# Kernel tuning notes

Hardware: AMD Instinct MI355X
Metric: run time of the kernel (lower is better)

Reference implementation:

```python
import jax, jax.numpy as jnp
import numpy as np

NUM_HEAD = 8
MSA_DIM = 256
PAIR_DIM = 128
KEY_DIM = MSA_DIM // NUM_HEAD  # 32 per-head dim
LN_EPS = 1e-5


def _layernorm(x, scale, offset):
    mu = jnp.mean(x, axis=-1, keepdims=True)
    var = jnp.var(x, axis=-1, keepdims=True)
    return (x - mu) * jax.lax.rsqrt(var + LN_EPS) * scale + offset


def setup_inputs() -> dict:
    key = jax.random.key(0)
    ks = jax.random.split(key, 16)
    S, R = 256, 256  # num sequences, num residues
    inp = {
        "msa_act": jax.random.normal(ks[0], (S, R, MSA_DIM), dtype=jnp.float32),
        "msa_mask": jnp.ones((S, R), dtype=jnp.int32),
        "pair_act": jax.random.normal(ks[1], (R, R, PAIR_DIM), dtype=jnp.float32),
        # LayerNorm params
        "qn_scale": jax.random.normal(ks[2], (MSA_DIM,), dtype=jnp.float32) * 0.02 + 1.0,
        "qn_offset": jax.random.normal(ks[3], (MSA_DIM,), dtype=jnp.float32) * 0.02,
        "pn_scale": jax.random.normal(ks[4], (PAIR_DIM,), dtype=jnp.float32) * 0.02 + 1.0,
        "pn_offset": jax.random.normal(ks[5], (PAIR_DIM,), dtype=jnp.float32) * 0.02,
        # pair-bias projection
        "feat_2d_weights": jax.random.normal(ks[6], (PAIR_DIM, NUM_HEAD), dtype=jnp.float32) * 0.1,
        # attention params
        "q_weights": jax.random.normal(ks[7], (MSA_DIM, NUM_HEAD, KEY_DIM), dtype=jnp.float32) * 0.05,
        "k_weights": jax.random.normal(ks[8], (MSA_DIM, NUM_HEAD, KEY_DIM), dtype=jnp.float32) * 0.05,
        "v_weights": jax.random.normal(ks[9], (MSA_DIM, NUM_HEAD, KEY_DIM), dtype=jnp.float32) * 0.05,
        "o_weights": jax.random.normal(ks[10], (NUM_HEAD, KEY_DIM, MSA_DIM), dtype=jnp.float32) * 0.05,
        "o_bias": jnp.zeros((MSA_DIM,), dtype=jnp.float32),
        "gating_w": jax.random.normal(ks[11], (MSA_DIM, NUM_HEAD, KEY_DIM), dtype=jnp.float32) * 0.05,
        "gating_b": jnp.ones((NUM_HEAD, KEY_DIM), dtype=jnp.float32),
    }
    return inp


def reference(msa_act, msa_mask, pair_act, qn_scale, qn_offset, pn_scale, pn_offset,
              feat_2d_weights, q_weights, k_weights, v_weights, o_weights, o_bias,
              gating_w, gating_b):
    # mask bias: [S, 1, 1, R]
    bias = (1e9 * (msa_mask.astype(jnp.float32) - 1.0))[:, None, None, :]
    m = _layernorm(msa_act, qn_scale, qn_offset)            # [S, R, C]
    p = _layernorm(pair_act, pn_scale, pn_offset)           # [R, R, Cz]
    nonbatched_bias = jnp.einsum('qkc,ch->hqk', p, feat_2d_weights)  # [H, R, R]

    q = jnp.einsum('bqa,ahc->bqhc', m, q_weights) * (KEY_DIM ** -0.5)
    k = jnp.einsum('bka,ahc->bkhc', m, k_weights)
    v = jnp.einsum('bka,ahc->bkhc', m, v_weights)
    logits = jnp.einsum('bqhc,bkhc->bhqk', q, k) + bias + nonbatched_bias[None]
    weights = jax.nn.softmax(logits, axis=-1)
    weighted_avg = jnp.einsum('bhqk,bkhc->bqhc', weights, v)

    gate = jax.nn.sigmoid(jnp.einsum('bqc,chv->bqhv', m, gating_w) + gating_b)
    weighted_avg = weighted_avg * gate

    out = jnp.einsum('bqhc,hco->bqo', weighted_avg, o_weights) + o_bias
    return out
```

## Files before the change

### kernel.cpp

```cpp
#include <hip/hip_runtime.h>
#include <hip/hip_bf16.h>
#include <stdint.h>


typedef unsigned short u16;
typedef unsigned int   u32;
typedef __attribute__((ext_vector_type(8))) short bf16x8;
typedef __attribute__((ext_vector_type(4))) float f32x4;

__device__ __forceinline__ float bf2f(u16 u){ union { u32 i; float f; } v; v.i = ((u32)u)<<16; return v.f; }
__device__ __forceinline__ u16 f2bf(float f){
  union { float f; u32 i; } v; v.f = f; u32 x = v.i;
  return (u16)((x + 0x7fffu + ((x>>16)&1u)) >> 16);
}
__device__ __forceinline__ u32 pk2(float a, float b){ return (u32)f2bf(a) | ((u32)f2bf(b) << 16); }

__device__ __forceinline__ void gl_lds16(const void* g, void* l){
  __builtin_amdgcn_global_load_lds(
    reinterpret_cast<const __attribute__((address_space(1))) unsigned int*>(reinterpret_cast<uintptr_t>(g)),
    reinterpret_cast<__attribute__((address_space(3))) unsigned int*>(reinterpret_cast<uintptr_t>(l)),
    16, 0, 0);
}

__global__ __launch_bounds__(256) void k_ln_msa(
    const float* __restrict__ x, const float* __restrict__ sc,
    const float* __restrict__ of, u16* __restrict__ mo)
{
  const int lane = threadIdx.x & 63;
  const int row  = (blockIdx.x << 2) + (threadIdx.x >> 6);
  float4 v = ((const float4*)(x + (size_t)row * 256))[lane];
  float s  = v.x + v.y + v.z + v.w;
  float s2 = v.x*v.x + v.y*v.y + v.z*v.z + v.w*v.w;
  #pragma unroll
  for (int o = 32; o > 0; o >>= 1){ s += __shfl_xor(s, o); s2 += __shfl_xor(s2, o); }
  const float mu = s * (1.0f/256.0f);
  const float rs = rsqrtf(s2 * (1.0f/256.0f) - mu*mu + 1e-5f);
  float4 scv = ((const float4*)sc)[lane];
  float4 ofv = ((const float4*)of)[lane];
  u32 p0 = pk2((v.x-mu)*rs*scv.x + ofv.x, (v.y-mu)*rs*scv.y + ofv.y);
  u32 p1 = pk2((v.z-mu)*rs*scv.z + ofv.z, (v.w-mu)*rs*scv.w + ofv.w);
  ((uint2*)(mo + (size_t)row * 256))[lane] = make_uint2(p0, p1);
}

__global__ __launch_bounds__(256) void k_ln_pair(
    const float* __restrict__ p, const float* __restrict__ sc,
    const float* __restrict__ of, const float* __restrict__ w2d,
    float* __restrict__ nb)
{
  const int lane = threadIdx.x & 63;
  const int row  = (blockIdx.x << 2) + (threadIdx.x >> 6);
  float2 v = ((const float2*)(p + (size_t)row * 128))[lane];
  float s = v.x + v.y, s2 = v.x*v.x + v.y*v.y;
  #pragma unroll
  for (int o = 32; o > 0; o >>= 1){ s += __shfl_xor(s, o); s2 += __shfl_xor(s2, o); }
  const float mu = s * (1.0f/128.0f);
  const float rs = rsqrtf(s2 * (1.0f/128.0f) - mu*mu + 1e-5f);
  const int c0 = lane * 2;
  const float y0 = (v.x - mu) * rs * sc[c0]     + of[c0];
  const float y1 = (v.y - mu) * rs * sc[c0 + 1] + of[c0 + 1];
  const float4* w0 = (const float4*)(w2d + c0 * 8);
  const float4* w1 = (const float4*)(w2d + (c0 + 1) * 8);
  float4 a0 = w0[0], b0 = w0[1], a1 = w1[0], b1 = w1[1];
  float ph[8];
  ph[0] = y0*a0.x + y1*a1.x; ph[1] = y0*a0.y + y1*a1.y;
  ph[2] = y0*a0.z + y1*a1.z; ph[3] = y0*a0.w + y1*a1.w;
  ph[4] = y0*b0.x + y1*b1.x; ph[5] = y0*b0.y + y1*b1.y;
  ph[6] = y0*b0.z + y1*b1.z; ph[7] = y0*b0.w + y1*b1.w;
  #pragma unroll
  for (int o = 32; o > 0; o >>= 1){
    #pragma unroll
    for (int hh = 0; hh < 8; hh++) ph[hh] += __shfl_xor(ph[hh], o);
  }
  if (lane == 0){
    #pragma unroll
    for (int hh = 0; hh < 8; hh++) nb[(size_t)hh * 65536 + row] = ph[hh];
  }
}

__global__ __launch_bounds__(256) void k_cast(
    const float* __restrict__ qw, const float* __restrict__ kw,
    const float* __restrict__ vw, const float* __restrict__ gw,
    const float* __restrict__ ow, u16* __restrict__ wT)
{
  const int mt = blockIdx.x >> 4;
  const float* src = (mt == 0) ? qw : (mt == 1) ? kw : (mt == 2) ? vw : (mt == 3) ? gw : ow;
  u16* dst = wT + mt * 65536;
  const int tid = threadIdx.x;
  const int n  = ((blockIdx.x & 15) << 4) + (tid & 15);
  const int kc = tid >> 4;
  float v[16];
  #pragma unroll
  for (int kk = 0; kk < 16; kk++) v[kk] = src[(kc*16 + kk)*256 + n];
  #pragma unroll
  for (int p = 0; p < 8; p++)
    *(u32*)&dst[n*256 + kc*16 + 2*p] = pk2(v[2*p], v[2*p+1]);
}

__global__ __launch_bounds__(256) void k_qkvg(
    const u16* __restrict__ m, const u16* __restrict__ wT, const float* __restrict__ gb,
    u16* __restrict__ qo, u16* __restrict__ ko, u16* __restrict__ vTo, u16* __restrict__ go)
{
  __shared__ __align__(16) u16 As[2][8192];
  __shared__ __align__(16) u16 Bs[2][8192];
  const int tid = threadIdx.x;
  const int w = tid >> 6, lane = tid & 63, g = lane >> 4, q16 = lane & 15;
  const int blk = blockIdx.x;
  const int bx = ((blk >> 6) << 3) | (blk & 7);
  const int by = (blk >> 3) & 7;
  const int row0  = bx << 7;
  const int mat   = by >> 1;
  const int ncol0 = (by & 1) << 7;
  const u16* Wt = wT + mat * 65536;
  const int wr = w >> 1, wc = w & 1;

  const int rA  = ((tid >> 7) << 4) + (tid & 15);
  const int kgA = (tid >> 4) & 7;

  const f32x4 z4 = {0.f, 0.f, 0.f, 0.f};
  f32x4 acc[4][4];
  #pragma unroll
  for (int i = 0; i < 4; i++)
    #pragma unroll
    for (int j = 0; j < 4; j++) acc[i][j] = z4;

  auto STAGE = [&](int buf, int ks){
    const int k0 = ks << 6;
    #pragma unroll
    for (int c = 0; c < 4; c++){
      gl_lds16(m  + (size_t)(row0  + rA + c*32)*256 + k0 + kgA*8,
               (char*)As + buf*16384 + c*4096 + w*1024);
      gl_lds16(Wt + (size_t)(ncol0 + rA + c*32)*256 + k0 + kgA*8,
               (char*)Bs + buf*16384 + c*4096 + w*1024);
    }
  };

  STAGE(0, 0);
  __syncthreads();

  #pragma unroll 1
  for (int ks = 0; ks < 4; ks++){
    const int cur = ks & 1;
    if (ks < 3) STAGE(cur ^ 1, ks + 1);
    const char* Ab = (const char*)As + cur*16384;
    const char* Bb = (const char*)Bs + cur*16384;
    #pragma unroll
    for (int kk = 0; kk < 2; kk++){
      bf16x8 af[4], bfr[4];
      #pragma unroll
      for (int i = 0; i < 4; i++){
        af[i]  = *(const bf16x8*)(Ab + (wr*4+i)*2048 + (kk*4+g)*256 + q16*16);
        bfr[i] = *(const bf16x8*)(Bb + (wc*4+i)*2048 + (kk*4+g)*256 + q16*16);
      }
      #pragma unroll
      for (int i = 0; i < 4; i++)
        #pragma unroll
        for (int j = 0; j < 4; j++)
          acc[i][j] = __builtin_amdgcn_mfma_f32_16x16x32_bf16(af[i], bfr[j], acc[i][j], 0, 0, 0);
    }
    if (ks < 3) __syncthreads();
  }

  const int b  = bx >> 1;
  const int rb = (row0 & 255) + wr*64 + 4*g;
  const int cb0 = ncol0 + wc*64 + q16;

  if (mat == 2){
    #pragma unroll
    for (int i = 0; i < 4; i++){
      const int r = rb + i*16;
      #pragma unroll
      for (int j = 0; j < 4; j++){
        const int col = cb0 + j*16;
        const int hh = col >> 5, cc = col & 31;
        u16* base = vTo + (size_t)(b*8 + hh)*8192 + cc*256 + r;
        *(u32*)base       = pk2(acc[i][j][0], acc[i][j][1]);
        *(u32*)(base + 2) = pk2(acc[i][j][2], acc[i][j][3]);
      }
    }
  } else {
    u16* O = (mat == 0) ? qo : (mat == 1) ? ko : go;
    #pragma unroll
    for (int i = 0; i < 4; i++){
      #pragma unroll
      for (int j = 0; j < 4; j++){
        const int col = cb0 + j*16;
        const int hh = col >> 5, cc = col & 31;
        f32x4 a = acc[i][j];
        if (mat == 0) a *= 0.17677669529663687f;
        #pragma unroll
        for (int v = 0; v < 4; v++){
          float x = a[v];
          if (mat == 3) x = 1.0f / (1.0f + __expf(-(x + gb[col])));
          O[(size_t)((b*8 + hh)*256 + rb + i*16 + v)*32 + cc] = f2bf(x);
        }
      }
    }
  }
}

__global__ __launch_bounds__(512, 4) void k_attn(
    const u16* __restrict__ qp, const u16* __restrict__ kp, const u16* __restrict__ vTp,
    const u16* __restrict__ gp, const int* __restrict__ mask, const float* __restrict__ nb,
    u16* __restrict__ gwa)
{
  __shared__ __align__(16) u16 Ksh[8192];
  __shared__ __align__(16) u16 Vsh[8192];
  __shared__ __align__(16) u16 Pb[8][2048];
  __shared__ float maskb[256];
  const int tid = threadIdx.x;
  const int w = tid >> 6, lane = tid & 63, g = lane >> 4, q16 = lane & 15;
  const int blk = blockIdx.x, b = blk >> 3, h = blk & 7;
  const size_t tb = (size_t)blk * 8192;

  #pragma unroll
  for (int c = 0; c < 2; c++){
    gl_lds16(kp  + tb + (size_t)((c*8 + w)*16 + q16)*32 + g*8,
             (char*)Ksh + c*8192 + w*1024);
    gl_lds16(vTp + tb + (size_t)(c*16 + q16)*256 + (w*4 + g)*8,
             (char*)Vsh + c*8192 + w*1024);
  }
  if (tid < 256) maskb[tid] = 1e9f * ((float)mask[b*256 + tid] - 1.0f);
  __syncthreads();

  const float* nbh = nb + (size_t)h * 65536;
  const f32x4 z4 = {0.f,0.f,0.f,0.f};
  u16* pb = Pb[w];
  const int rsw = (g ^ (q16 & 3)) << 4;

  #pragma unroll 1
  for (int jj = 0; jj < 2; jj++){
    const int q = w*32 + jj*16 + q16;
    const bf16x8 qf = *(const bf16x8*)(qp + tb + (size_t)q*32 + g*8);
    f32x4 O0 = z4, O1 = z4;
    float l = 0.f, mrun = -3.0e38f;

    #pragma unroll 1
    for (int hh = 0; hh < 2; hh++){
      f32x4 S[8];
      #pragma unroll
      for (int n8 = 0; n8 < 8; n8++){
        const bf16x8 kf = *(const bf16x8*)((const char*)Ksh + (hh*8+n8)*1024 + g*256 + q16*16);
        S[n8] = __builtin_amdgcn_mfma_f32_16x16x32_bf16(kf, qf, z4, 0, 0, 0);
      }
      float hmax = -3.0e38f;
      #pragma unroll
      for (int n8 = 0; n8 < 8; n8++){
        const f32x4 nbv = *(const f32x4*)(nbh + (size_t)q*256 + (hh*8+n8)*16 + 4*g);
        const f32x4 mbv = *(const f32x4*)&maskb[(hh*8+n8)*16 + 4*g];
        S[n8] += nbv + mbv;
        hmax = fmaxf(hmax, fmaxf(fmaxf(S[n8][0],S[n8][1]), fmaxf(S[n8][2],S[n8][3])));
      }
      hmax = fmaxf(hmax, __shfl_xor(hmax, 16));
      hmax = fmaxf(hmax, __shfl_xor(hmax, 32));
      const float mnew = fmaxf(mrun, hmax);
      const float fsc = __expf(mrun - mnew);
      l *= fsc; O0 *= fsc; O1 *= fsc; mrun = mnew;

      u32 cpk[8], dpk[8];
      #pragma unroll
      for (int n8 = 0; n8 < 8; n8++){
        const float p0 = __expf(S[n8][0]-mnew), p1 = __expf(S[n8][1]-mnew);
        const float p2 = __expf(S[n8][2]-mnew), p3 = __expf(S[n8][3]-mnew);
        l += (p0+p1)+(p2+p3);
        cpk[n8] = pk2(p0,p1); dpk[n8] = pk2(p2,p3);
      }
      #pragma unroll
      for (int n8 = 0; n8 < 8; n8++){
        const int sl = (2*(n8&1) + (g>>1)) ^ (q16&3);
        *(uint2*)((char*)pb + (n8>>1)*1024 + q16*64 + sl*16 + (g&1)*8)
            = make_uint2(cpk[n8], dpk[n8]);
      }
      #pragma unroll
      for (int c4 = 0; c4 < 4; c4++){
        const bf16x8 pf = *(const bf16x8*)((const char*)pb + c4*1024 + q16*64 + rsw);
        const int kg = (hh*4 + c4)*4 + g;
        const bf16x8 v0 = *(const bf16x8*)((const char*)Vsh + kg*256 + q16*16);
        const bf16x8 v1 = *(const bf16x8*)((const char*)Vsh + 8192 + kg*256 + q16*16);
        O0 = __builtin_amdgcn_mfma_f32_16x16x32_bf16(v0, pf, O0, 0, 0, 0);
        O1 = __builtin_amdgcn_mfma_f32_16x16x32_bf16(v1, pf, O1, 0, 0, 0);
      }
    }

    l += __shfl_xor(l, 16);
    l += __shfl_xor(l, 32);
    const float inv = 1.0f / l;

    const uint2 gvA = *(const uint2*)(gp + tb + (size_t)q*32 + 4*g);
    const uint2 gvB = *(const uint2*)(gp + tb + (size_t)q*32 + 16 + 4*g);
    const float ga0 = bf2f((u16)(gvA.x & 0xffffu)), ga1 = bf2f((u16)(gvA.x >> 16));
    const float ga2 = bf2f((u16)(gvA.y & 0xffffu)), ga3 = bf2f((u16)(gvA.y >> 16));
    const float gb0 = bf2f((u16)(gvB.x & 0xffffu)), gb1 = bf2f((u16)(gvB.x >> 16));
    const float gb2 = bf2f((u16)(gvB.y & 0xffffu)), gb3 = bf2f((u16)(gvB.y >> 16));
    u16* dst = gwa + (size_t)(b*256 + q)*256 + h*32 + 4*g;
    *(u32*)dst        = pk2(O0[0]*inv*ga0, O0[1]*inv*ga1);
    *(u32*)(dst + 2)  = pk2(O0[2]*inv*ga2, O0[3]*inv*ga3);
    *(u32*)(dst + 16) = pk2(O1[0]*inv*gb0, O1[1]*inv*gb1);
    *(u32*)(dst + 18) = pk2(O1[2]*inv*gb2, O1[3]*inv*gb3);
  }
}

__global__ __launch_bounds__(256) void k_out(
    const u16* __restrict__ a, const u16* __restrict__ Wt, const float* __restrict__ ob,
    float* __restrict__ out)
{
  __shared__ __align__(16) u16 As[2][8192];
  __shared__ __align__(16) u16 Bs[2][8192];
  const int tid = threadIdx.x;
  const int w = tid >> 6, lane = tid & 63, g = lane >> 4, q16 = lane & 15;
  const int blk = blockIdx.x;
  const int bx = ((blk >> 4) << 3) | (blk & 7);
  const int by = (blk >> 3) & 1;
  const int row0  = bx << 7;
  const int ncol0 = by << 7;
  const int wr = w >> 1, wc = w & 1;

  const int rA  = ((tid >> 7) << 4) + (tid & 15);
  const int kgA = (tid >> 4) & 7;

  const f32x4 z4 = {0.f, 0.f, 0.f, 0.f};
  f32x4 acc[4][4];
  #pragma unroll
  for (int i = 0; i < 4; i++)
    #pragma unroll
    for (int j = 0; j < 4; j++) acc[i][j] = z4;

  auto STAGE = [&](int buf, int ks){
    const int k0 = ks << 6;
    #pragma unroll
    for (int c = 0; c < 4; c++){
      gl_lds16(a  + (size_t)(row0  + rA + c*32)*256 + k0 + kgA*8,
               (char*)As + buf*16384 + c*4096 + w*1024);
      gl_lds16(Wt + (size_t)(ncol0 + rA + c*32)*256 + k0 + kgA*8,
               (char*)Bs + buf*16384 + c*4096 + w*1024);
    }
  };

  STAGE(0, 0);
  __syncthreads();

  #pragma unroll 1
  for (int ks = 0; ks < 4; ks++){
    const int cur = ks & 1;
    if (ks < 3) STAGE(cur ^ 1, ks + 1);
    const char* Ab = (const char*)As + cur*16384;
    const char* Bb = (const char*)Bs + cur*16384;
    #pragma unroll
    for (int kk = 0; kk < 2; kk++){
      bf16x8 af[4], bfr[4];
      #pragma unroll
      for (int i = 0; i < 4; i++){
        af[i]  = *(const bf16x8*)(Ab + (wr*4+i)*2048 + (kk*4+g)*256 + q16*16);
        bfr[i] = *(const bf16x8*)(Bb + (wc*4+i)*2048 + (kk*4+g)*256 + q16*16);
      }
      #pragma unroll
      for (int i = 0; i < 4; i++)
        #pragma unroll
        for (int j = 0; j < 4; j++)
          acc[i][j] = __builtin_amdgcn_mfma_f32_16x16x32_bf16(af[i], bfr[j], acc[i][j], 0, 0, 0);
    }
    if (ks < 3) __syncthreads();
  }

  const int rb = row0 + wr*64 + 4*g;
  #pragma unroll
  for (int i = 0; i < 4; i++){
    #pragma unroll
    for (int j = 0; j < 4; j++){
      const int col = ncol0 + wc*64 + j*16 + q16;
      const float bias = ob[col];
      #pragma unroll
      for (int v = 0; v < 4; v++)
        out[(size_t)(rb + i*16 + v)*256 + col] = acc[i][j][v] + bias;
    }
  }
}

extern "C" void kernel_launch(void* const* d_in, const int* in_sizes, int n_in,
                              void* d_out, int out_size, void* d_ws, size_t ws_size,
                              hipStream_t stream)
{
  (void)in_sizes; (void)n_in; (void)out_size; (void)ws_size;
  const float* msa  = (const float*)d_in[0];
  const int*   mask = (const int*)  d_in[1];
  const float* pair = (const float*)d_in[2];
  const float* qns  = (const float*)d_in[3];
  const float* qno  = (const float*)d_in[4];
  const float* pns  = (const float*)d_in[5];
  const float* pno  = (const float*)d_in[6];
  const float* w2d  = (const float*)d_in[7];
  const float* qw   = (const float*)d_in[8];
  const float* kw   = (const float*)d_in[9];
  const float* vw   = (const float*)d_in[10];
  const float* ow   = (const float*)d_in[11];
  const float* ob   = (const float*)d_in[12];
  const float* gw   = (const float*)d_in[13];
  const float* gb   = (const float*)d_in[14];
  float* out = (float*)d_out;

  char* ws = (char*)d_ws;
  u16*   m_ws = (u16*)ws;
  float* nb   = (float*)(ws + 33554432);
  u16*   q_ws = (u16*)(ws + 35651584);
  u16*   k_ws = q_ws + 16777216;
  u16*   vT_ws= k_ws + 16777216;
  u16*   g_ws = vT_ws + 16777216;
  u16*   wT   = (u16*)(ws + 169869312);
  u16*   gwa  = m_ws;

  k_ln_msa <<<16384, 256, 0, stream>>>(msa, qns, qno, m_ws);
  k_ln_pair<<<16384, 256, 0, stream>>>(pair, pns, pno, w2d, nb);
  k_cast   <<<   80, 256, 0, stream>>>(qw, kw, vw, gw, ow, wT);
  k_qkvg   <<< 4096, 256, 0, stream>>>(m_ws, wT, gb, q_ws, k_ws, vT_ws, g_ws);
  k_attn   <<< 2048, 512, 0, stream>>>(q_ws, k_ws, vT_ws, g_ws, mask, nb, gwa);
  k_out    <<< 1024, 256, 0, stream>>>(gwa, wT + 4*65536, ob, out);
}
```

Before: 440.2 us.

## Halve GEMM K-tile and swap MFMA operands for vectorized row-major stores

The projection and output GEMMs now stage 32-wide K slices instead of 64, halving LDS per block and doubling the number of pipeline steps. For the q/k/gate and output paths, the MFMA operands are swapped so each lane holds four consecutive columns, which allows 8-byte bf16 and 16-byte float4 global stores in place of scalar scattered stores. The V-transpose store is merged into a single uint2 write. The smaller LDS footprint may raise occupancy, at the cost of twice as many barriers per K loop.

Measured after the change: 417.8 us. 1.05x faster.

```diff
diff --git a/kernel.cpp b/kernel.cpp
--- a/kernel.cpp
+++ b/kernel.cpp
@@ -100,8 +100,8 @@
     const u16* __restrict__ m, const u16* __restrict__ wT, const float* __restrict__ gb,
     u16* __restrict__ qo, u16* __restrict__ ko, u16* __restrict__ vTo, u16* __restrict__ go)
 {
-  __shared__ __align__(16) u16 As[2][8192];
-  __shared__ __align__(16) u16 Bs[2][8192];
+  __shared__ __align__(16) u16 As[2][4096];
+  __shared__ __align__(16) u16 Bs[2][4096];
   const int tid = threadIdx.x;
   const int w = tid >> 6, lane = tid & 63, g = lane >> 4, q16 = lane & 15;
   const int blk = blockIdx.x;
@@ -113,9 +113,6 @@
   const u16* Wt = wT + mat * 65536;
   const int wr = w >> 1, wc = w & 1;
 
-  const int rA  = ((tid >> 7) << 4) + (tid & 15);
-  const int kgA = (tid >> 4) & 7;
-
   const f32x4 z4 = {0.f, 0.f, 0.f, 0.f};
   f32x4 acc[4][4];
   #pragma unroll
@@ -124,47 +121,39 @@
     for (int j = 0; j < 4; j++) acc[i][j] = z4;
 
   auto STAGE = [&](int buf, int ks){
-    const int k0 = ks << 6;
-    #pragma unroll
-    for (int c = 0; c < 4; c++){
-      gl_lds16(m  + (size_t)(row0  + rA + c*32)*256 + k0 + kgA*8,
-               (char*)As + buf*16384 + c*4096 + w*1024);
-      gl_lds16(Wt + (size_t)(ncol0 + rA + c*32)*256 + k0 + kgA*8,
-               (char*)Bs + buf*16384 + c*4096 + w*1024);
+    const int k0 = ks << 5;
+    #pragma unroll
+    for (int c = 0; c < 2; c++){
+      const int rr = (c*4 + w)*16 + q16;
+      gl_lds16(m  + (size_t)(row0  + rr)*256 + k0 + g*8, (char*)As[buf] + (c*4+w)*1024);
+      gl_lds16(Wt + (size_t)(ncol0 + rr)*256 + k0 + g*8, (char*)Bs[buf] + (c*4+w)*1024);
     }
   };
 
   STAGE(0, 0);
   __syncthreads();
 
-  #pragma unroll 1
-  for (int ks = 0; ks < 4; ks++){
-    const int cur = ks & 1;
-    if (ks < 3) STAGE(cur ^ 1, ks + 1);
-    const char* Ab = (const char*)As + cur*16384;
-    const char* Bb = (const char*)Bs + cur*16384;
-    #pragma unroll
-    for (int kk = 0; kk < 2; kk++){
+  if (mat == 2){
+    #pragma unroll 1
+    for (int ks = 0; ks < 8; ks++){
+      const int cur = ks & 1;
+      if (ks < 7) STAGE(cur ^ 1, ks + 1);
       bf16x8 af[4], bfr[4];
       #pragma unroll
       for (int i = 0; i < 4; i++){
-        af[i]  = *(const bf16x8*)(Ab + (wr*4+i)*2048 + (kk*4+g)*256 + q16*16);
-        bfr[i] = *(const bf16x8*)(Bb + (wc*4+i)*2048 + (kk*4+g)*256 + q16*16);
+        af[i]  = *(const bf16x8*)((const char*)As[cur] + (wr*4+i)*1024 + g*256 + q16*16);
+        bfr[i] = *(const bf16x8*)((const char*)Bs[cur] + (wc*4+i)*1024 + g*256 + q16*16);
       }
       #pragma unroll
       for (int i = 0; i < 4; i++)
         #pragma unroll
         for (int j = 0; j < 4; j++)
           acc[i][j] = __builtin_amdgcn_mfma_f32_16x16x32_bf16(af[i], bfr[j], acc[i][j], 0, 0, 0);
-    }
-    if (ks < 3) __syncthreads();
-  }
-
-  const int b  = bx >> 1;
-  const int rb = (row0 & 255) + wr*64 + 4*g;
-  const int cb0 = ncol0 + wc*64 + q16;
-
-  if (mat == 2){
+      if (ks < 7) __syncthreads();
+    }
+    const int b  = bx >> 1;
+    const int rb = (row0 & 255) + wr*64 + 4*g;
+    const int cb0 = ncol0 + wc*64 + q16;
     #pragma unroll
     for (int i = 0; i < 4; i++){
       const int r = rb + i*16;
@@ -173,26 +162,46 @@
         const int col = cb0 + j*16;
         const int hh = col >> 5, cc = col & 31;
         u16* base = vTo + (size_t)(b*8 + hh)*8192 + cc*256 + r;
-        *(u32*)base       = pk2(acc[i][j][0], acc[i][j][1]);
-        *(u32*)(base + 2) = pk2(acc[i][j][2], acc[i][j][3]);
+        *(uint2*)base = make_uint2(pk2(acc[i][j][0], acc[i][j][1]),
+                                   pk2(acc[i][j][2], acc[i][j][3]));
       }
     }
   } else {
+    #pragma unroll 1
+    for (int ks = 0; ks < 8; ks++){
+      const int cur = ks & 1;
+      if (ks < 7) STAGE(cur ^ 1, ks + 1);
+      bf16x8 af[4], bfr[4];
+      #pragma unroll
+      for (int i = 0; i < 4; i++){
+        af[i]  = *(const bf16x8*)((const char*)As[cur] + (wr*4+i)*1024 + g*256 + q16*16);
+        bfr[i] = *(const bf16x8*)((const char*)Bs[cur] + (wc*4+i)*1024 + g*256 + q16*16);
+      }
+      #pragma unroll
+      for (int i = 0; i < 4; i++)
+        #pragma unroll
+        for (int j = 0; j < 4; j++)
+          acc[i][j] = __builtin_amdgcn_mfma_f32_16x16x32_bf16(bfr[j], af[i], acc[i][j], 0, 0, 0);
+      if (ks < 7) __syncthreads();
+    }
     u16* O = (mat == 0) ? qo : (mat == 1) ? ko : go;
+    const int b = bx >> 1;
     #pragma unroll
     for (int i = 0; i < 4; i++){
+      const int row = (row0 & 255) + (wr*4 + i)*16 + q16;
       #pragma unroll
       for (int j = 0; j < 4; j++){
-        const int col = cb0 + j*16;
+        const int col = ncol0 + wc*64 + j*16 + 4*g;
         const int hh = col >> 5, cc = col & 31;
         f32x4 a = acc[i][j];
         if (mat == 0) a *= 0.17677669529663687f;
-        #pragma unroll
-        for (int v = 0; v < 4; v++){
-          float x = a[v];
-          if (mat == 3) x = 1.0f / (1.0f + __expf(-(x + gb[col])));
-          O[(size_t)((b*8 + hh)*256 + rb + i*16 + v)*32 + cc] = f2bf(x);
+        else if (mat == 3){
+          #pragma unroll
+          for (int v = 0; v < 4; v++)
+            a[v] = 1.0f / (1.0f + __expf(-(a[v] + gb[col + v])));
         }
+        u16* dst = O + ((size_t)(b*8 + hh)*256 + row)*32 + cc;
+        *(uint2*)dst = make_uint2(pk2(a[0], a[1]), pk2(a[2], a[3]));
       }
     }
   }
@@ -303,8 +312,8 @@
     const u16* __restrict__ a, const u16* __restrict__ Wt, const float* __restrict__ ob,
     float* __restrict__ out)
 {
-  __shared__ __align__(16) u16 As[2][8192];
-  __shared__ __align__(16) u16 Bs[2][8192];
+  __shared__ __align__(16) u16 As[2][4096];
+  __shared__ __align__(16) u16 Bs[2][4096];
   const int tid = threadIdx.x;
   const int w = tid >> 6, lane = tid & 63, g = lane >> 4, q16 = lane & 15;
   const int blk = blockIdx.x;
@@ -314,9 +323,6 @@
   const int ncol0 = by << 7;
   const int wr = w >> 1, wc = w & 1;
 
-  const int rA  = ((tid >> 7) << 4) + (tid & 15);
-  const int kgA = (tid >> 4) & 7;
-
   const f32x4 z4 = {0.f, 0.f, 0.f, 0.f};
   f32x4 acc[4][4];
   #pragma unroll
@@ -325,13 +331,12 @@
     for (int j = 0; j < 4; j++) acc[i][j] = z4;
 
   auto STAGE = [&](int buf, int ks){
-    const int k0 = ks << 6;
-    #pragma unroll
-    for (int c = 0; c < 4; c++){
-      gl_lds16(a  + (size_t)(row0  + rA + c*32)*256 + k0 + kgA*8,
-               (char*)As + buf*16384 + c*4096 + w*1024);
-      gl_lds16(Wt + (size_t)(ncol0 + rA + c*32)*256 + k0 + kgA*8,
-               (char*)Bs + buf*16384 + c*4096 + w*1024);
+    const int k0 = ks << 5;
+    #pragma unroll
+    for (int c = 0; c < 2; c++){
+      const int rr = (c*4 + w)*16 + q16;
+      gl_lds16(a  + (size_t)(row0  + rr)*256 + k0 + g*8, (char*)As[buf] + (c*4+w)*1024);
+      gl_lds16(Wt + (size_t)(ncol0 + rr)*256 + k0 + g*8, (char*)Bs[buf] + (c*4+w)*1024);
     }
   };
 
@@ -339,38 +344,33 @@
   __syncthreads();
 
   #pragma unroll 1
-  for (int ks = 0; ks < 4; ks++){
+  for (int ks = 0; ks < 8; ks++){
     const int cur = ks & 1;
-    if (ks < 3) STAGE(cur ^ 1, ks + 1);
-    const char* Ab = (const char*)As + cur*16384;
-    const char* Bb = (const char*)Bs + cur*16384;
-    #pragma unroll
-    for (int kk = 0; kk < 2; kk++){
-      bf16x8 af[4], bfr[4];
-      #pragma unroll
-      for (int i = 0; i < 4; i++){
-        af[i]  = *(const bf16x8*)(Ab + (wr*4+i)*2048 + (kk*4+g)*256 + q16*16);
-        bfr[i] = *(const bf16x8*)(Bb + (wc*4+i)*2048 + (kk*4+g)*256 + q16*16);
-      }
-      #pragma unroll
-      for (int i = 0; i < 4; i++)
-        #pragma unroll
-        for (int j = 0; j < 4; j++)
-          acc[i][j] = __builtin_amdgcn_mfma_f32_16x16x32_bf16(af[i], bfr[j], acc[i][j], 0, 0, 0);
-    }
-    if (ks < 3) __syncthreads();
-  }
-
-  const int rb = row0 + wr*64 + 4*g;
+    if (ks < 7) STAGE(cur ^ 1, ks + 1);
+    bf16x8 af[4], bfr[4];
+    #pragma unroll
+    for (int i = 0; i < 4; i++){
+      af[i]  = *(const bf16x8*)((const char*)As[cur] + (wr*4+i)*1024 + g*256 + q16*16);
+      bfr[i] = *(const bf16x8*)((const char*)Bs[cur] + (wc*4+i)*1024 + g*256 + q16*16);
+    }
+    #pragma unroll
+    for (int i = 0; i < 4; i++)
+      #pragma unroll
+      for (int j = 0; j < 4; j++)
+        acc[i][j] = __builtin_amdgcn_mfma_f32_16x16x32_bf16(bfr[j], af[i], acc[i][j], 0, 0, 0);
+    if (ks < 7) __syncthreads();
+  }
+
   #pragma unroll
   for (int i = 0; i < 4; i++){
+    const int row = row0 + (wr*4 + i)*16 + q16;
     #pragma unroll
     for (int j = 0; j < 4; j++){
-      const int col = ncol0 + wc*64 + j*16 + q16;
-      const float bias = ob[col];
-      #pragma unroll
-      for (int v = 0; v < 4; v++)
-        out[(size_t)(rb + i*16 + v)*256 + col] = acc[i][j][v] + bias;
+      const int col = ncol0 + wc*64 + j*16 + 4*g;
+      const float4 bv = *(const float4*)&ob[col];
+      f32x4 acv = acc[i][j];
+      *(float4*)&out[(size_t)row*256 + col] =
+          make_float4(acv[0]+bv.x, acv[1]+bv.y, acv[2]+bv.z, acv[3]+bv.w);
     }
   }
 }
```
